# Optimization experiments

Measured on AMD Instinct MI355X. Metric: run time of the kernel, lower is better.

The kernel has to match this reference:

```python
import jax, jax.numpy as jnp
import numpy as np

N, IN_DIM, OUT_DIM, HEADS = 8192, 256, 256, 2
C = OUT_DIM // HEADS  # per-head channel dim (concat=True)
ALPHA = 0.2
NEG = -9e15


def setup_inputs() -> dict:
    key = jax.random.key(0)
    ks = jax.random.split(key, 9)
    h = jax.random.normal(ks[0], (N, IN_DIM), dtype=jnp.float32)
    adj = jax.random.randint(ks[1], (N, N), 0, 2, dtype=jnp.int32)
    # torch nn.Linear weights are [out, in]; xavier-like scale
    def xav(k, shape):
        fan_in, fan_out = shape[1], shape[0]
        s = 1.414 * np.sqrt(6.0 / (fan_in + fan_out))
        return jax.random.uniform(k, shape, jnp.float32, -s, s)
    W1 = xav(ks[2], (HEADS * C, IN_DIM))
    W2 = xav(ks[3], (HEADS * C, IN_DIM))
    W3 = xav(ks[4], (HEADS * C, IN_DIM))
    b1 = jnp.zeros((HEADS * C,), jnp.float32)
    b2 = jnp.zeros((HEADS * C,), jnp.float32)
    b3 = jnp.zeros((HEADS * C,), jnp.float32)
    sa = 1.414 * np.sqrt(6.0 / (HEADS + 2 * C))
    a = jax.random.uniform(ks[5], (HEADS, 2 * C), jnp.float32, -sa, sa)
    return {"h": h, "adj": adj, "W1": W1, "b1": b1, "W2": W2, "b2": b2,
            "W3": W3, "b3": b3, "a": a}


def reference(h, adj, W1, b1, W2, b2, W3, b3, a):
    n = h.shape[0]
    W1h = (h @ W1.T + b1).reshape(n, HEADS, C)  # [N,H,C]
    W2h = (h @ W2.T + b2).reshape(n, HEADS, C)
    W3h = (h @ W3.T + b3).reshape(n, HEADS, C)
    # eij = a . [W1h_i || W2h_j] decomposes into per-node scores
    a1, a2 = a[:, :C], a[:, C:]
    s1 = jnp.einsum('nhc,hc->nh', W1h, a1)  # [N,H]
    s2 = jnp.einsum('nhc,hc->nh', W2h, a2)  # [N,H]
    e = jax.nn.leaky_relu(s1[:, None, :] + s2[None, :, :], ALPHA)  # [N,N,H]
    e = jnp.where(adj[:, :, None] == 1, e, NEG)
    att = jax.nn.softmax(e, axis=1)  # softmax over source dim j (dim=1)
    # dropout is identity in eval mode (training=False)
    h_prime = jnp.einsum('ijh,jhc->ihc', att, W3h)  # [N,H,C]
    return h_prime.reshape(n, HEADS * C)
```

## Files before the change

kernel.cpp:

```cpp
#include <hip/hip_runtime.h>
#include <hip/hip_bf16.h>

#define NN 8192
#define LOG2E 1.44269504088896f
#define S_SPLIT 8
#define JC 1024
#define NT 32

typedef __attribute__((ext_vector_type(8))) short short8;
typedef __attribute__((ext_vector_type(4))) float f32x4;

static __device__ __forceinline__ float bf2f(unsigned short u) {
    union { unsigned int i; float f; } v; v.i = ((unsigned int)u) << 16; return v.f;
}
static __device__ __forceinline__ unsigned short f2bf(float f) {
    union { float f; unsigned int i; } v; v.f = f;
    unsigned int lsb = (v.i >> 16) & 1u;
    v.i += 0x7fffu + lsb;
    return (unsigned short)(v.i >> 16);
}
static __device__ __forceinline__ unsigned int cvtpk(float lo, float hi) {
    unsigned int r;
    asm("v_cvt_pk_bf16_f32 %0, %1, %2" : "=v"(r) : "v"(lo), "v"(hi));
    return r;
}
static __device__ __forceinline__ float fexp2(float x) { return __builtin_amdgcn_exp2f(x); }

static __device__ __forceinline__ void cvt8(const float* __restrict__ p, short8& hi, short8& lo) {
    float4 u = *(const float4*)p;
    float4 v = *(const float4*)(p + 4);
    float f[8] = {u.x, u.y, u.z, u.w, v.x, v.y, v.z, v.w};
#pragma unroll
    for (int j = 0; j < 8; ++j) {
        unsigned short hb = f2bf(f[j]);
        hi[j] = (short)hb;
        lo[j] = (short)f2bf(f[j] - bf2f(hb));
    }
}

__global__ __launch_bounds__(256) void pack_kernel(const int* __restrict__ adj,
                                                   unsigned int* __restrict__ abits) {
    int w = blockIdx.x * 256 + threadIdx.x;
    const int* src = adj + (size_t)w * 32;
    unsigned int bits = 0;
#pragma unroll
    for (int k = 0; k < 8; ++k) {
        int4 v = *(const int4*)(src + k * 4);
        bits |= (unsigned int)(v.x & 1) << (k * 4 + 0);
        bits |= (unsigned int)(v.y & 1) << (k * 4 + 1);
        bits |= (unsigned int)(v.z & 1) << (k * 4 + 2);
        bits |= (unsigned int)(v.w & 1) << (k * 4 + 3);
    }
    abits[w] = bits;
}

__global__ void prep_partial(const float* __restrict__ W1, const float* __restrict__ W2,
                             const float* __restrict__ a,
                             float* __restrict__ v1p, float* __restrict__ v2p) {
    int b = blockIdx.x;
    int t = threadIdx.x;
    int hh = t >> 8, k = t & 255;
    int c0 = (b & 7) * 16;
    const float* W = (b < 8) ? W1 : W2;
    int aoff = (b < 8) ? 0 : 128;
    float acc = 0.f;
    for (int c = c0; c < c0 + 16; ++c)
        acc += W[(size_t)(hh * 128 + c) * 256 + k] * a[hh * 256 + aoff + c];
    ((b < 8) ? v1p : v2p)[(b & 7) * 512 + t] = acc;
}

__global__ void prep_reduce(const float* __restrict__ b1, const float* __restrict__ b2,
                            const float* __restrict__ a,
                            const float* __restrict__ v1p, const float* __restrict__ v2p,
                            float* __restrict__ v1, float* __restrict__ v2, float* __restrict__ bd) {
    int t = threadIdx.x;
    float a1 = 0.f, a2 = 0.f;
    for (int b = 0; b < 8; ++b) { a1 += v1p[b * 512 + t]; a2 += v2p[b * 512 + t]; }
    v1[t] = a1;
    v2[t] = a2;
    int g = t >> 7;
    int hh = g >> 1, which = g & 1, c = t & 127;
    float prod = which ? b2[hh * 128 + c] * a[hh * 256 + 128 + c]
                       : b1[hh * 128 + c] * a[hh * 256 + c];
#pragma unroll
    for (int off = 1; off < 64; off <<= 1) prod += __shfl_xor(prod, off);
    __shared__ float ws[8];
    if ((t & 63) == 0) ws[t >> 6] = prod;
    __syncthreads();
    if (t < 4) bd[t] = ws[2 * t] + ws[2 * t + 1];
}

__global__ __launch_bounds__(256) void s_kernel(const float* __restrict__ hmat,
                         const float* __restrict__ v1, const float* __restrict__ v2,
                         const float* __restrict__ bd,
                         float* __restrict__ s1o, float* __restrict__ s2o) {
    int w = threadIdx.x >> 6, l = threadIdx.x & 63;
    int n = blockIdx.x * 4 + w;
    float4 hv  = *(const float4*)(hmat + (size_t)n * 256 + l * 4);
    float4 va0 = *(const float4*)(v1 + l * 4);
    float4 va1 = *(const float4*)(v1 + 256 + l * 4);
    float4 vb0 = *(const float4*)(v2 + l * 4);
    float4 vb1 = *(const float4*)(v2 + 256 + l * 4);
    float s10 = hv.x*va0.x + hv.y*va0.y + hv.z*va0.z + hv.w*va0.w;
    float s11 = hv.x*va1.x + hv.y*va1.y + hv.z*va1.z + hv.w*va1.w;
    float s20 = hv.x*vb0.x + hv.y*vb0.y + hv.z*vb0.z + hv.w*vb0.w;
    float s21 = hv.x*vb1.x + hv.y*vb1.y + hv.z*vb1.z + hv.w*vb1.w;
#pragma unroll
    for (int off = 1; off < 64; off <<= 1) {
        s10 += __shfl_xor(s10, off);
        s11 += __shfl_xor(s11, off);
        s20 += __shfl_xor(s20, off);
        s21 += __shfl_xor(s21, off);
    }
    if (l == 0) {
        s1o[n*2 + 0] = (s10 + bd[0]) * LOG2E;
        s1o[n*2 + 1] = (s11 + bd[2]) * LOG2E;
        s2o[n]       = (s20 + bd[1]) * LOG2E;
        s2o[NN + n]  = (s21 + bd[3]) * LOG2E;
    }
}

__global__ void wcvt_kernel(const float* __restrict__ W3,
                            unsigned short* __restrict__ w3hi, unsigned short* __restrict__ w3lo) {
    int i = blockIdx.x * 256 + threadIdx.x;
    float f = W3[i];
    unsigned short hb = f2bf(f);
    w3hi[i] = hb;
    w3lo[i] = f2bf(f - bf2f(hb));
}

__global__ __launch_bounds__(256) void w3_kernel(const float* __restrict__ hmat,
                                                 const unsigned short* __restrict__ w3hi,
                                                 const unsigned short* __restrict__ w3lo,
                                                 const float* __restrict__ b3,
                                                 unsigned short* __restrict__ w3b) {
    int tid = threadIdx.x;
    int w = tid >> 6, l = tid & 63;
    int m = l & 15, kq = l >> 4;
    int n0 = (blockIdx.x * 2 + (w & 1)) * 16;
    int c0 = (w >> 1) * 8;
    f32x4 acc[8];
#pragma unroll
    for (int ct = 0; ct < 8; ++ct) acc[ct] = (f32x4){0.f, 0.f, 0.f, 0.f};
    for (int k0 = 0; k0 < 256; k0 += 32) {
        short8 ahi, alo;
        cvt8(hmat + (size_t)(n0 + m) * 256 + k0 + kq * 8, ahi, alo);
#pragma unroll
        for (int ct = 0; ct < 8; ++ct) {
            int c = (c0 + ct) * 16 + m;
            short8 bhi = *(const short8*)&w3hi[(size_t)c * 256 + k0 + kq * 8];
            short8 blo = *(const short8*)&w3lo[(size_t)c * 256 + k0 + kq * 8];
            acc[ct] = __builtin_amdgcn_mfma_f32_16x16x32_bf16(ahi, bhi, acc[ct], 0, 0, 0);
            acc[ct] = __builtin_amdgcn_mfma_f32_16x16x32_bf16(alo, bhi, acc[ct], 0, 0, 0);
            acc[ct] = __builtin_amdgcn_mfma_f32_16x16x32_bf16(ahi, blo, acc[ct], 0, 0, 0);
        }
    }
#pragma unroll
    for (int ct = 0; ct < 8; ++ct) {
        int c = (c0 + ct) * 16 + m;
        float bias = b3[c];
#pragma unroll
        for (int e = 0; e < 4; ++e) {
            int n = n0 + kq * 4 + e;
            size_t idx = ((size_t)(n >> 5) * 16 + (c >> 4)) * 512 + (size_t)((((n >> 3) & 3) * 16 + m) * 8 + (n & 7));
            w3b[idx] = f2bf(acc[ct][e] + bias);
        }
    }
}

__global__ __launch_bounds__(256, 6) void attn_fused(
        const unsigned int* __restrict__ abits, const float* __restrict__ s1a,
        const float* __restrict__ s2h, const unsigned short* __restrict__ w3b,
        unsigned short* __restrict__ pacc, float* __restrict__ pden)
{
    __shared__ unsigned short Pt[2][32][32];
    __shared__ float s2t[2][JC];

    const int tid = threadIdx.x;
    const int wv = tid >> 6, ln = tid & 63;
    const int m = ln & 15, kq = ln >> 4;
    const int hw = wv >> 1;
    const int r = tid >> 3, oct = tid & 7;
    const int i0 = blockIdx.x * 32;
    const int sidx = blockIdx.y;
    const int j0 = sidx * JC;
    const int sw = kq ^ ((m >> 1) & 3);

    const float s1r0 = s1a[(i0 + r) * 2 + 0];
    const float s1r1 = s1a[(i0 + r) * 2 + 1];
    const unsigned int* abR = abits + (size_t)(i0 + r) * 256 + (j0 >> 5);
    unsigned short* ptw = &Pt[0][0][0] + r * 32 + ((((oct >> 1) ^ ((r >> 1) & 3)) << 3) | ((oct & 1) << 2));
    const unsigned short* pta = &Pt[hw][m][0] + (sw << 3);
    const unsigned short* w3p = w3b + ((size_t)(j0 >> 5) * 16 + wv * 4) * 512 + ln * 8;

    f32x4 acc[2][4];
    f32x4 accd[2];
#pragma unroll
    for (int rt = 0; rt < 2; ++rt) {
        accd[rt] = (f32x4){0.f, 0.f, 0.f, 0.f};
#pragma unroll
        for (int f = 0; f < 4; ++f) acc[rt][f] = (f32x4){0.f, 0.f, 0.f, 0.f};
    }
    short8 ones;
#pragma unroll
    for (int e = 0; e < 8; ++e) ones[e] = (short)0x3F80;

    for (int x = tid; x < 2 * JC; x += 256) {
        int h = x >> 10, j = x & (JC - 1);
        s2t[h][j] = s2h[(size_t)h * NN + j0 + j];
    }
    unsigned int cur = abR[0];
    __syncthreads();

    for (int t = 0; t < NT; ++t) {
        const unsigned short* bp = w3p + (size_t)t * 8192;
        short8 bf0 = *(const short8*)(bp);
        short8 bf1 = *(const short8*)(bp + 512);
        short8 bf2 = *(const short8*)(bp + 1024);
        short8 bf3 = *(const short8*)(bp + 1536);
        unsigned int nxt = abR[(t + 1 < NT) ? t + 1 : t];
        {
            unsigned int sh = cur >> (oct * 4);
            float4 sv0 = *(const float4*)&s2t[0][t * 32 + oct * 4];
            float4 sv1 = *(const float4*)&s2t[1][t * 32 + oct * 4];
            float x0, q0, q1, q2, q3, u0, u1, u2, u3;
            x0 = s1r0 + sv0.x; x0 = fmaxf(x0, 0.2f * x0); q0 = (sh & 1u) ? fexp2(x0) : 0.f;
            x0 = s1r0 + sv0.y; x0 = fmaxf(x0, 0.2f * x0); q1 = (sh & 2u) ? fexp2(x0) : 0.f;
            x0 = s1r0 + sv0.z; x0 = fmaxf(x0, 0.2f * x0); q2 = (sh & 4u) ? fexp2(x0) : 0.f;
            x0 = s1r0 + sv0.w; x0 = fmaxf(x0, 0.2f * x0); q3 = (sh & 8u) ? fexp2(x0) : 0.f;
            x0 = s1r1 + sv1.x; x0 = fmaxf(x0, 0.2f * x0); u0 = (sh & 1u) ? fexp2(x0) : 0.f;
            x0 = s1r1 + sv1.y; x0 = fmaxf(x0, 0.2f * x0); u1 = (sh & 2u) ? fexp2(x0) : 0.f;
            x0 = s1r1 + sv1.z; x0 = fmaxf(x0, 0.2f * x0); u2 = (sh & 4u) ? fexp2(x0) : 0.f;
            x0 = s1r1 + sv1.w; x0 = fmaxf(x0, 0.2f * x0); u3 = (sh & 8u) ? fexp2(x0) : 0.f;
            uint2 w0 = {cvtpk(q0, q1), cvtpk(q2, q3)};
            uint2 w1 = {cvtpk(u0, u1), cvtpk(u2, u3)};
            *(uint2*)ptw = w0;
            *(uint2*)(ptw + 1024) = w1;
        }
        asm volatile("s_waitcnt lgkmcnt(0)" ::: "memory");
        __builtin_amdgcn_sched_barrier(0);
        __builtin_amdgcn_s_barrier();
        asm volatile("" ::: "memory");
        {
            short8 a0 = *(const short8*)pta;
            short8 a1 = *(const short8*)(pta + 512);
            __builtin_amdgcn_s_setprio(1);
            acc[0][0] = __builtin_amdgcn_mfma_f32_16x16x32_bf16(a0, bf0, acc[0][0], 0, 0, 0);
            acc[1][0] = __builtin_amdgcn_mfma_f32_16x16x32_bf16(a1, bf0, acc[1][0], 0, 0, 0);
            acc[0][1] = __builtin_amdgcn_mfma_f32_16x16x32_bf16(a0, bf1, acc[0][1], 0, 0, 0);
            acc[1][1] = __builtin_amdgcn_mfma_f32_16x16x32_bf16(a1, bf1, acc[1][1], 0, 0, 0);
            acc[0][2] = __builtin_amdgcn_mfma_f32_16x16x32_bf16(a0, bf2, acc[0][2], 0, 0, 0);
            acc[1][2] = __builtin_amdgcn_mfma_f32_16x16x32_bf16(a1, bf2, acc[1][2], 0, 0, 0);
            acc[0][3] = __builtin_amdgcn_mfma_f32_16x16x32_bf16(a0, bf3, acc[0][3], 0, 0, 0);
            acc[1][3] = __builtin_amdgcn_mfma_f32_16x16x32_bf16(a1, bf3, acc[1][3], 0, 0, 0);
            if ((wv & 1) == 0) {
                accd[0] = __builtin_amdgcn_mfma_f32_16x16x32_bf16(a0, ones, accd[0], 0, 0, 0);
                accd[1] = __builtin_amdgcn_mfma_f32_16x16x32_bf16(a1, ones, accd[1], 0, 0, 0);
            }
            __builtin_amdgcn_s_setprio(0);
        }
        asm volatile("" ::: "memory");
        __builtin_amdgcn_s_barrier();
        asm volatile("" ::: "memory");
        cur = nxt;
    }

    if ((wv & 1) == 0 && m == 0) {
#pragma unroll
        for (int rt = 0; rt < 2; ++rt)
#pragma unroll
            for (int e = 0; e < 4; ++e) {
                int row = i0 + rt * 16 + kq * 4 + e;
                pden[((size_t)sidx * NN + row) * 2 + hw] = accd[rt][e];
            }
    }
    size_t pb_ = (size_t)sidx * NN * 256;
#pragma unroll
    for (int rt = 0; rt < 2; ++rt)
#pragma unroll
        for (int e = 0; e < 4; ++e) {
            int row = i0 + rt * 16 + kq * 4 + e;
#pragma unroll
            for (int f = 0; f < 4; ++f) {
                int col = wv * 64 + f * 16 + m;
                pacc[pb_ + (size_t)row * 256 + col] = f2bf(acc[rt][f][e]);
            }
        }
}

__global__ void combine_kernel(const unsigned short* __restrict__ pacc, const float* __restrict__ pden,
                               float* __restrict__ out) {
    size_t idx = ((size_t)blockIdx.x * 256 + threadIdx.x) * 8;
    int i = (int)(idx >> 8);
    int c = (int)(idx & 255);
    int hh = c >> 7;
    float acc[8];
#pragma unroll
    for (int e = 0; e < 8; ++e) acc[e] = 0.f;
    float den = 0.f;
    for (int s = 0; s < S_SPLIT; ++s) {
        uint4 v = *(const uint4*)&pacc[(size_t)s * NN * 256 + idx];
        unsigned int uu[4] = {v.x, v.y, v.z, v.w};
#pragma unroll
        for (int q = 0; q < 4; ++q) {
            acc[2*q]   += bf2f((unsigned short)(uu[q] & 0xffff));
            acc[2*q+1] += bf2f((unsigned short)(uu[q] >> 16));
        }
        den += pden[((size_t)s * NN + i) * 2 + hh];
    }
    float r = 1.f / den;
    float4 o0 = {acc[0]*r, acc[1]*r, acc[2]*r, acc[3]*r};
    float4 o1 = {acc[4]*r, acc[5]*r, acc[6]*r, acc[7]*r};
    *(float4*)&out[idx] = o0;
    *(float4*)&out[idx + 4] = o1;
}

extern "C" void kernel_launch(void* const* d_in, const int* in_sizes, int n_in,
                              void* d_out, int out_size, void* d_ws, size_t ws_size,
                              hipStream_t stream) {
    const float* hmat = (const float*)d_in[0];
    const int*   adj  = (const int*)d_in[1];
    const float* W1   = (const float*)d_in[2];
    const float* b1   = (const float*)d_in[3];
    const float* W2   = (const float*)d_in[4];
    const float* b2   = (const float*)d_in[5];
    const float* W3   = (const float*)d_in[6];
    const float* b3   = (const float*)d_in[7];
    const float* a    = (const float*)d_in[8];
    float* out = (float*)d_out;

    char* p = (char*)d_ws;
    float* v1   = (float*)p; p += 2048;
    float* v2   = (float*)p; p += 2048;
    float* bd   = (float*)p; p += 256;
    float* s1   = (float*)p; p += (size_t)NN * 2 * sizeof(float);
    float* s2h  = (float*)p; p += (size_t)NN * 2 * sizeof(float);
    float* v1p  = (float*)p; p += 8 * 512 * sizeof(float);
    float* v2p  = (float*)p; p += 8 * 512 * sizeof(float);
    unsigned short* w3hi = (unsigned short*)p; p += 65536 * 2;
    unsigned short* w3lo = (unsigned short*)p; p += 65536 * 2;
    unsigned short* w3b  = (unsigned short*)p; p += (size_t)NN * 256 * 2;
    unsigned int* abits  = (unsigned int*)p;   p += (size_t)NN * (NN / 32) / 8 * sizeof(unsigned int) * 8;
    float* pden = (float*)p; p += (size_t)S_SPLIT * NN * 2 * sizeof(float);
    unsigned short* pacc = (unsigned short*)p;

    pack_kernel<<<(NN * (NN / 32)) / 256, 256, 0, stream>>>(adj, abits);
    prep_partial<<<16, 512, 0, stream>>>(W1, W2, a, v1p, v2p);
    prep_reduce<<<1, 512, 0, stream>>>(b1, b2, a, v1p, v2p, v1, v2, bd);
    s_kernel<<<NN / 4, 256, 0, stream>>>(hmat, v1, v2, bd, s1, s2h);
    wcvt_kernel<<<256, 256, 0, stream>>>(W3, w3hi, w3lo);
    w3_kernel<<<256, 256, 0, stream>>>(hmat, w3hi, w3lo, b3, w3b);
    attn_fused<<<dim3(NN / 32, S_SPLIT), 256, 0, stream>>>(abits, s1, s2h, w3b, pacc, pden);
    combine_kernel<<<(NN * 256) / (256 * 8), 256, 0, stream>>>(pacc, pden, out);
}
```

Measured before the change: 160.3 us.

## Fuse adjacency packing into attention kernel with 64-row blocks and double-buffered P

Removes the separate bit-packing kernel and has the attention kernel read the int32 adjacency matrix directly, using nontemporal loads prefetched two tiles ahead. Blocks grow to 512 threads covering 64 rows so each W3 tile load serves twice as many rows. The P tile in shared memory is double-buffered, which drops the second barrier per iteration. In exchange the attention kernel now streams the full 256MB adjacency matrix itself instead of a packed bitmask, and per-thread register pressure from prefetching may limit occupancy.

```diff
diff --git a/kernel.cpp b/kernel.cpp
--- a/kernel.cpp
+++ b/kernel.cpp
@@ -9,6 +9,7 @@
 
 typedef __attribute__((ext_vector_type(8))) short short8;
 typedef __attribute__((ext_vector_type(4))) float f32x4;
+typedef __attribute__((ext_vector_type(4))) int int4v;
 
 static __device__ __forceinline__ float bf2f(unsigned short u) {
     union { unsigned int i; float f; } v; v.i = ((unsigned int)u) << 16; return v.f;
@@ -36,22 +37,6 @@
         hi[j] = (short)hb;
         lo[j] = (short)f2bf(f[j] - bf2f(hb));
     }
-}
-
-__global__ __launch_bounds__(256) void pack_kernel(const int* __restrict__ adj,
-                                                   unsigned int* __restrict__ abits) {
-    int w = blockIdx.x * 256 + threadIdx.x;
-    const int* src = adj + (size_t)w * 32;
-    unsigned int bits = 0;
-#pragma unroll
-    for (int k = 0; k < 8; ++k) {
-        int4 v = *(const int4*)(src + k * 4);
-        bits |= (unsigned int)(v.x & 1) << (k * 4 + 0);
-        bits |= (unsigned int)(v.y & 1) << (k * 4 + 1);
-        bits |= (unsigned int)(v.z & 1) << (k * 4 + 2);
-        bits |= (unsigned int)(v.w & 1) << (k * 4 + 3);
-    }
-    abits[w] = bits;
 }
 
 __global__ void prep_partial(const float* __restrict__ W1, const float* __restrict__ W2,
@@ -168,30 +153,31 @@
     }
 }
 
-__global__ __launch_bounds__(256, 6) void attn_fused(
-        const unsigned int* __restrict__ abits, const float* __restrict__ s1a,
+__global__ __launch_bounds__(512, 4) void attn_fused(
+        const int* __restrict__ adj, const float* __restrict__ s1a,
         const float* __restrict__ s2h, const unsigned short* __restrict__ w3b,
         unsigned short* __restrict__ pacc, float* __restrict__ pden)
 {
-    __shared__ unsigned short Pt[2][32][32];
+    __shared__ unsigned short Pt[2][2][64][32];
     __shared__ float s2t[2][JC];
 
     const int tid = threadIdx.x;
     const int wv = tid >> 6, ln = tid & 63;
     const int m = ln & 15, kq = ln >> 4;
-    const int hw = wv >> 1;
+    const int rg = wv & 1, cg = wv >> 1;
+    const int hw = cg >> 1;
     const int r = tid >> 3, oct = tid & 7;
-    const int i0 = blockIdx.x * 32;
+    const int i0 = blockIdx.x * 64;
     const int sidx = blockIdx.y;
     const int j0 = sidx * JC;
     const int sw = kq ^ ((m >> 1) & 3);
 
     const float s1r0 = s1a[(i0 + r) * 2 + 0];
     const float s1r1 = s1a[(i0 + r) * 2 + 1];
-    const unsigned int* abR = abits + (size_t)(i0 + r) * 256 + (j0 >> 5);
-    unsigned short* ptw = &Pt[0][0][0] + r * 32 + ((((oct >> 1) ^ ((r >> 1) & 3)) << 3) | ((oct & 1) << 2));
-    const unsigned short* pta = &Pt[hw][m][0] + (sw << 3);
-    const unsigned short* w3p = w3b + ((size_t)(j0 >> 5) * 16 + wv * 4) * 512 + ln * 8;
+    const int* adjRow = adj + (size_t)(i0 + r) * NN + j0 + oct * 4;
+    unsigned short* ptw = &Pt[0][0][0][0] + r * 32 + ((((oct >> 1) ^ ((r >> 1) & 3)) << 3) | ((oct & 1) << 2));
+    const unsigned short* pta = &Pt[0][0][0][0] + (size_t)hw * 2048 + (rg * 32 + m) * 32 + (sw << 3);
+    const unsigned short* w3p = w3b + ((size_t)(j0 >> 5) * 16 + cg * 4) * 512 + ln * 8;
 
     f32x4 acc[2][4];
     f32x4 accd[2];
@@ -205,45 +191,49 @@
 #pragma unroll
     for (int e = 0; e < 8; ++e) ones[e] = (short)0x3F80;
 
-    for (int x = tid; x < 2 * JC; x += 256) {
+    for (int x = tid; x < 2 * JC; x += 512) {
         int h = x >> 10, j = x & (JC - 1);
         s2t[h][j] = s2h[(size_t)h * NN + j0 + j];
     }
-    unsigned int cur = abR[0];
+    int4v aCur = __builtin_nontemporal_load((const int4v*)(adjRow));
+    int4v aNxt = __builtin_nontemporal_load((const int4v*)(adjRow + 32));
     __syncthreads();
 
     for (int t = 0; t < NT; ++t) {
+        const int buf = t & 1;
         const unsigned short* bp = w3p + (size_t)t * 8192;
         short8 bf0 = *(const short8*)(bp);
         short8 bf1 = *(const short8*)(bp + 512);
         short8 bf2 = *(const short8*)(bp + 1024);
         short8 bf3 = *(const short8*)(bp + 1536);
-        unsigned int nxt = abR[(t + 1 < NT) ? t + 1 : t];
+        int tn2 = (t + 2 < NT) ? t + 2 : NT - 1;
+        int4v aNew = __builtin_nontemporal_load((const int4v*)(adjRow + tn2 * 32));
         {
-            unsigned int sh = cur >> (oct * 4);
             float4 sv0 = *(const float4*)&s2t[0][t * 32 + oct * 4];
             float4 sv1 = *(const float4*)&s2t[1][t * 32 + oct * 4];
             float x0, q0, q1, q2, q3, u0, u1, u2, u3;
-            x0 = s1r0 + sv0.x; x0 = fmaxf(x0, 0.2f * x0); q0 = (sh & 1u) ? fexp2(x0) : 0.f;
-            x0 = s1r0 + sv0.y; x0 = fmaxf(x0, 0.2f * x0); q1 = (sh & 2u) ? fexp2(x0) : 0.f;
-            x0 = s1r0 + sv0.z; x0 = fmaxf(x0, 0.2f * x0); q2 = (sh & 4u) ? fexp2(x0) : 0.f;
-            x0 = s1r0 + sv0.w; x0 = fmaxf(x0, 0.2f * x0); q3 = (sh & 8u) ? fexp2(x0) : 0.f;
-            x0 = s1r1 + sv1.x; x0 = fmaxf(x0, 0.2f * x0); u0 = (sh & 1u) ? fexp2(x0) : 0.f;
-            x0 = s1r1 + sv1.y; x0 = fmaxf(x0, 0.2f * x0); u1 = (sh & 2u) ? fexp2(x0) : 0.f;
-            x0 = s1r1 + sv1.z; x0 = fmaxf(x0, 0.2f * x0); u2 = (sh & 4u) ? fexp2(x0) : 0.f;
-            x0 = s1r1 + sv1.w; x0 = fmaxf(x0, 0.2f * x0); u3 = (sh & 8u) ? fexp2(x0) : 0.f;
+            x0 = s1r0 + sv0.x; x0 = fmaxf(x0, 0.2f * x0); q0 = aCur.x ? fexp2(x0) : 0.f;
+            x0 = s1r0 + sv0.y; x0 = fmaxf(x0, 0.2f * x0); q1 = aCur.y ? fexp2(x0) : 0.f;
+            x0 = s1r0 + sv0.z; x0 = fmaxf(x0, 0.2f * x0); q2 = aCur.z ? fexp2(x0) : 0.f;
+            x0 = s1r0 + sv0.w; x0 = fmaxf(x0, 0.2f * x0); q3 = aCur.w ? fexp2(x0) : 0.f;
+            x0 = s1r1 + sv1.x; x0 = fmaxf(x0, 0.2f * x0); u0 = aCur.x ? fexp2(x0) : 0.f;
+            x0 = s1r1 + sv1.y; x0 = fmaxf(x0, 0.2f * x0); u1 = aCur.y ? fexp2(x0) : 0.f;
+            x0 = s1r1 + sv1.z; x0 = fmaxf(x0, 0.2f * x0); u2 = aCur.z ? fexp2(x0) : 0.f;
+            x0 = s1r1 + sv1.w; x0 = fmaxf(x0, 0.2f * x0); u3 = aCur.w ? fexp2(x0) : 0.f;
             uint2 w0 = {cvtpk(q0, q1), cvtpk(q2, q3)};
             uint2 w1 = {cvtpk(u0, u1), cvtpk(u2, u3)};
-            *(uint2*)ptw = w0;
-            *(uint2*)(ptw + 1024) = w1;
+            unsigned short* pw = ptw + buf * 4096;
+            *(uint2*)pw = w0;
+            *(uint2*)(pw + 2048) = w1;
         }
         asm volatile("s_waitcnt lgkmcnt(0)" ::: "memory");
         __builtin_amdgcn_sched_barrier(0);
         __builtin_amdgcn_s_barrier();
         asm volatile("" ::: "memory");
         {
-            short8 a0 = *(const short8*)pta;
-            short8 a1 = *(const short8*)(pta + 512);
+            const unsigned short* pa = pta + buf * 4096;
+            short8 a0 = *(const short8*)pa;
+            short8 a1 = *(const short8*)(pa + 512);
             __builtin_amdgcn_s_setprio(1);
             acc[0][0] = __builtin_amdgcn_mfma_f32_16x16x32_bf16(a0, bf0, acc[0][0], 0, 0, 0);
             acc[1][0] = __builtin_amdgcn_mfma_f32_16x16x32_bf16(a1, bf0, acc[1][0], 0, 0, 0);
@@ -253,24 +243,21 @@
             acc[1][2] = __builtin_amdgcn_mfma_f32_16x16x32_bf16(a1, bf2, acc[1][2], 0, 0, 0);
             acc[0][3] = __builtin_amdgcn_mfma_f32_16x16x32_bf16(a0, bf3, acc[0][3], 0, 0, 0);
             acc[1][3] = __builtin_amdgcn_mfma_f32_16x16x32_bf16(a1, bf3, acc[1][3], 0, 0, 0);
-            if ((wv & 1) == 0) {
+            if ((cg & 1) == 0) {
                 accd[0] = __builtin_amdgcn_mfma_f32_16x16x32_bf16(a0, ones, accd[0], 0, 0, 0);
                 accd[1] = __builtin_amdgcn_mfma_f32_16x16x32_bf16(a1, ones, accd[1], 0, 0, 0);
             }
             __builtin_amdgcn_s_setprio(0);
         }
-        asm volatile("" ::: "memory");
-        __builtin_amdgcn_s_barrier();
-        asm volatile("" ::: "memory");
-        cur = nxt;
-    }
-
-    if ((wv & 1) == 0 && m == 0) {
+        aCur = aNxt; aNxt = aNew;
+    }
+
+    if ((cg & 1) == 0 && m == 0) {
 #pragma unroll
         for (int rt = 0; rt < 2; ++rt)
 #pragma unroll
             for (int e = 0; e < 4; ++e) {
-                int row = i0 + rt * 16 + kq * 4 + e;
+                int row = i0 + rg * 32 + rt * 16 + kq * 4 + e;
                 pden[((size_t)sidx * NN + row) * 2 + hw] = accd[rt][e];
             }
     }
@@ -279,11 +266,11 @@
     for (int rt = 0; rt < 2; ++rt)
 #pragma unroll
         for (int e = 0; e < 4; ++e) {
-            int row = i0 + rt * 16 + kq * 4 + e;
+            int row = i0 + rg * 32 + rt * 16 + kq * 4 + e;
 #pragma unroll
             for (int f = 0; f < 4; ++f) {
-                int col = wv * 64 + f * 16 + m;
-                pacc[pb_ + (size_t)row * 256 + col] = f2bf(acc[rt][f][e]);
+                int col = cg * 64 + f * 16 + m;
+                __builtin_nontemporal_store(f2bf(acc[rt][f][e]), &pacc[pb_ + (size_t)row * 256 + col]);
             }
         }
 }
@@ -340,16 +327,14 @@
     unsigned short* w3hi = (unsigned short*)p; p += 65536 * 2;
     unsigned short* w3lo = (unsigned short*)p; p += 65536 * 2;
     unsigned short* w3b  = (unsigned short*)p; p += (size_t)NN * 256 * 2;
-    unsigned int* abits  = (unsigned int*)p;   p += (size_t)NN * (NN / 32) / 8 * sizeof(unsigned int) * 8;
     float* pden = (float*)p; p += (size_t)S_SPLIT * NN * 2 * sizeof(float);
     unsigned short* pacc = (unsigned short*)p;
 
-    pack_kernel<<<(NN * (NN / 32)) / 256, 256, 0, stream>>>(adj, abits);
     prep_partial<<<16, 512, 0, stream>>>(W1, W2, a, v1p, v2p);
     prep_reduce<<<1, 512, 0, stream>>>(b1, b2, a, v1p, v2p, v1, v2, bd);
     s_kernel<<<NN / 4, 256, 0, stream>>>(hmat, v1, v2, bd, s1, s2h);
     wcvt_kernel<<<256, 256, 0, stream>>>(W3, w3hi, w3lo);
     w3_kernel<<<256, 256, 0, stream>>>(hmat, w3hi, w3lo, b3, w3b);
-    attn_fused<<<dim3(NN / 32, S_SPLIT), 256, 0, stream>>>(abits, s1, s2h, w3b, pacc, pden);
+    attn_fused<<<dim3(NN / 64, S_SPLIT), 512, 0, stream>>>(adj, s1, s2h, w3b, pacc, pden);
     combine_kernel<<<(NN * 256) / (256 * 8), 256, 0, stream>>>(pacc, pden, out);
 }
```

Result: slower. 172.1 us (+7.3%).
